# Performance work log

Hardware: AMD Instinct MI355X
Metric: run time of the kernel (lower is better)

## Reference

```python
import jax, jax.numpy as jnp
import numpy as np

GRID_SIZE = 5
SPLINE_ORDER = 3
NUM_COEFF = GRID_SIZE + SPLINE_ORDER  # 8
L = 3
B, I, H = 4096, 256, 512
EPS = 1e-5


def make_grid(in_features):
    # efficient-kan default grid over [-1, 1] extended by spline_order knots each side
    h = 2.0 / GRID_SIZE
    g = jnp.arange(-SPLINE_ORDER, GRID_SIZE + SPLINE_ORDER + 1, dtype=jnp.float32) * h - 1.0
    return jnp.broadcast_to(g, (in_features, g.shape[0]))  # (in, G+2k+1)


def b_splines(x, grid):
    # x: (B, in), grid: (in, G+2k+1) -> (B, in, G+k) via Cox-de-Boor recursion
    xg = x[..., None]
    bases = ((xg >= grid[:, :-1]) & (xg < grid[:, 1:])).astype(x.dtype)
    for j in range(1, SPLINE_ORDER + 1):
        left = (xg - grid[:, :-(j + 1)]) / (grid[:, j:-1] - grid[:, :-(j + 1)])
        right = (grid[:, j + 1:] - xg) / (grid[:, j + 1:] - grid[:, 1:-j])
        bases = left * bases[..., :-1] + right * bases[..., 1:]
    return bases


def kan_linear(x, base_w, spline_w, grid):
    # base path: SiLU(x) @ W_base^T ; spline path: sum over (in, coeff)
    base = jax.nn.silu(x) @ base_w.T
    spl = jnp.einsum('bik,oik->bo', b_splines(x, grid), spline_w)
    return base + spl


def layer_norm(x, g, b):
    mu = jnp.mean(x, axis=-1, keepdims=True)
    var = jnp.var(x, axis=-1, keepdims=True)
    return (x - mu) / jnp.sqrt(var + EPS) * g + b


def _sublayer(z_prev, wx_b, wx_s, wh_b, wh_s, hz_b, hz_s, phi_b, phi_s,
              hh_w, hh_b, ln_g, ln_b, x_t, grid_in, grid_h):
    s_t = kan_linear(x_t, wx_b, wx_s, grid_in) + kan_linear(z_prev, wh_b, wh_s, grid_h)
    o_t = kan_linear(s_t, phi_b, phi_s, grid_h)
    z_t = layer_norm(z_prev @ hh_w.T + hh_b + kan_linear(o_t, hz_b, hz_s, grid_h), ln_g, ln_b)
    return o_t, z_t


def setup_inputs() -> dict:
    key = jax.random.key(0)
    ks = jax.random.split(key, 24)
    s = 0.05  # small init to keep gates/splines in sane range
    inp = {
        'x_t': jax.random.normal(ks[0], (B, I), jnp.float32),
        'h_prev': jax.random.normal(ks[1], (B, H), jnp.float32),
        'c_prev': jax.random.normal(ks[2], (B, H), jnp.float32),
        'z_prev': jax.random.normal(ks[3], (L, B, H), jnp.float32),
        'wx_base': jax.random.normal(ks[4], (L, H, I), jnp.float32) * s,
        'wx_spline': jax.random.normal(ks[5], (L, H, I, NUM_COEFF), jnp.float32) * s,
        'wh_base': jax.random.normal(ks[6], (L, H, H), jnp.float32) * s,
        'wh_spline': jax.random.normal(ks[7], (L, H, H, NUM_COEFF), jnp.float32) * s,
        'hz_base': jax.random.normal(ks[8], (L, H, H), jnp.float32) * s,
        'hz_spline': jax.random.normal(ks[9], (L, H, H, NUM_COEFF), jnp.float32) * s,
        'phi_base': jax.random.normal(ks[10], (L, H, H), jnp.float32) * s,
        'phi_spline': jax.random.normal(ks[11], (L, H, H, NUM_COEFF), jnp.float32) * s,
        'hh_w': jax.random.normal(ks[12], (L, H, H), jnp.float32) * s,
        'hh_b': jax.random.normal(ks[13], (L, H), jnp.float32) * s,
        'ln_g': jnp.ones((L, H), jnp.float32),
        'ln_b': jnp.zeros((L, H), jnp.float32),
        'f_w': jax.random.normal(ks[14], (H, I + H), jnp.float32) * s,
        'f_b': jax.random.normal(ks[15], (H,), jnp.float32) * s,
        'i_w': jax.random.normal(ks[16], (H, I + H), jnp.float32) * s,
        'i_b': jax.random.normal(ks[17], (H,), jnp.float32) * s,
        'g_w': jax.random.normal(ks[18], (H, I + H), jnp.float32) * s,
        'g_b': jax.random.normal(ks[19], (H,), jnp.float32) * s,
        'o_w': jax.random.normal(ks[20], (H, L * H), jnp.float32) * s,
        'o_b': jax.random.normal(ks[21], (H,), jnp.float32) * s,
    }
    return inp


def reference(x_t, h_prev, c_prev, z_prev, wx_base, wx_spline, wh_base, wh_spline,
              hz_base, hz_spline, phi_base, phi_spline, hh_w, hh_b, ln_g, ln_b,
              f_w, f_b, i_w, i_b, g_w, g_b, o_w, o_b):
    grid_in = make_grid(I)
    grid_h = make_grid(H)
    cat = jnp.concatenate([x_t, h_prev], axis=-1)  # (B, I+H)
    f_t = jax.nn.sigmoid(cat @ f_w.T + f_b)
    i_t = jax.nn.sigmoid(cat @ i_w.T + i_b)
    g_t = jnp.tanh(cat @ g_w.T + g_b)
    # vmap the RKAN sublayer over the L stacked sublayers
    sub = jax.vmap(_sublayer, in_axes=(0,) * 13 + (None, None, None))
    o_all, z_all = sub(z_prev, wx_base, wx_spline, wh_base, wh_spline,
                       hz_base, hz_spline, phi_base, phi_spline,
                       hh_w, hh_b, ln_g, ln_b, x_t, grid_in, grid_h)
    # concat sublayer phi outputs: (L,B,H) -> (B, L*H)
    r_t = jnp.transpose(o_all, (1, 0, 2)).reshape(B, L * H)
    o_t = jax.nn.sigmoid(r_t @ o_w.T + o_b)
    c_t = f_t * c_prev + i_t * g_t
    h_t = o_t * jnp.tanh(c_t)
    return h_t, c_t, z_all
```

## Files before the change

kernel.cpp:

```cpp
#include <hip/hip_runtime.h>

typedef __attribute__((ext_vector_type(8))) short short8;
typedef __attribute__((ext_vector_type(4))) float floatx4;

__device__ inline short f2bf(float v) {
    unsigned u = __builtin_bit_cast(unsigned, v);
    unsigned r = (u + 0x7fffu + ((u >> 16) & 1u)) >> 16;
    return (short)r;
}
__device__ inline float bf2f(short s) {
    unsigned u = ((unsigned)(unsigned short)s) << 16;
    return __builtin_bit_cast(float, u);
}

__device__ inline void spline8(float v, short* arr) {
    float u = (v + 2.2f) * 2.5f;
    float fj = floorf(u);
    int jj = (int)fj;
    float t1 = u - fj;
    float ok = (jj >= 0 && jj <= 10) ? (1.f / 6.f) : 0.f;
    float t2 = t1 * t1, t3 = t2 * t1;
    float omt = 1.f - t1;
    short sw0 = f2bf(omt * omt * omt * ok);
    short sw1 = f2bf((3.f * t3 - 6.f * t2 + 4.f) * ok);
    short sw2 = f2bf((-3.f * t3 + 3.f * t2 + 3.f * t1 + 1.f) * ok);
    short sw3 = f2bf(t3 * ok);
#pragma unroll
    for (int s = 0; s < 8; ++s) {
        int rr = s - jj + 3;
        arr[s] = (rr == 0) ? sw0 : (rr == 1) ? sw1 : (rr == 2) ? sw2
                 : (rr == 3) ? sw3 : (short)0;
    }
}

__global__ __launch_bounds__(256) void gemm64(
    int swz,
    const short* __restrict__ A0, int lda0, long sA0, int K0,
    const short* __restrict__ W0, int ldw0, long sW0,
    const short* __restrict__ A1, int lda1, long sA1, int K1,
    const short* __restrict__ W1, int ldw1, long sW1,
    short* __restrict__ C, int ldc, long sC)
{
    __shared__ short As[64 * 32];
    __shared__ short Ws[128 * 32];
    const int t = threadIdx.x;
    int bxi = blockIdx.x, byi = blockIdx.y, bzi = blockIdx.z;
    if (swz) {
        int n = bxi + (byi << 6) + (bzi << 8);
        int k = n & 7, j = n >> 3;
        byi = j & 3;
        bxi = k * 8 + ((j >> 2) & 7);
        bzi = j >> 5;
    }
    const int z = bzi;
    const int bm = bxi * 64;
    const int bn = byi * 128;
    const int lane = t & 63, w = t >> 6;
    const int wm = (w >> 1) * 32, wn = (w & 1) * 64;
    const int lrow = lane & 15, quad = lane >> 4;

    floatx4 acc[2][4] = {};

    const short* A = A0 + (long)z * sA0;
    const short* W = W0 + (long)z * sW0;
    int K = K0, lda = lda0, ldw = ldw0;

    for (int seg = 0; seg < 2; ++seg) {
        for (int k0 = 0; k0 < K; k0 += 32) {
            {
                int row = t >> 2, cg = (t & 3) * 8;
                const short* gp = A + (long)(bm + row) * lda + k0 + cg;
                __builtin_amdgcn_global_load_lds(
                    (const __attribute__((address_space(1))) void*)gp,
                    (__attribute__((address_space(3))) void*)(As + t * 8), 16, 0, 0);
            }
#pragma unroll
            for (int j = 0; j < 2; ++j) {
                int cj = j * 256 + t;
                int row = cj >> 2, cg = (cj & 3) * 8;
                const short* gq = W + (long)(bn + row) * ldw + k0 + cg;
                __builtin_amdgcn_global_load_lds(
                    (const __attribute__((address_space(1))) void*)gq,
                    (__attribute__((address_space(3))) void*)(Ws + cj * 8), 16, 0, 0);
            }
            __syncthreads();
            short8 af[2], bfr[4];
#pragma unroll
            for (int mi = 0; mi < 2; ++mi)
                af[mi] = *(const short8*)(As + (wm + mi * 16 + lrow) * 32 + quad * 8);
#pragma unroll
            for (int ni = 0; ni < 4; ++ni)
                bfr[ni] = *(const short8*)(Ws + (wn + ni * 16 + lrow) * 32 + quad * 8);
#pragma unroll
            for (int mi = 0; mi < 2; ++mi)
#pragma unroll
                for (int ni = 0; ni < 4; ++ni)
                    acc[mi][ni] = __builtin_amdgcn_mfma_f32_16x16x32_bf16(
                        af[mi], bfr[ni], acc[mi][ni], 0, 0, 0);
            __syncthreads();
        }
        A = A1 + (long)z * sA1; W = W1 + (long)z * sW1;
        K = K1; lda = lda1; ldw = ldw1;
    }

    short* Cz = C + (long)z * sC;
#pragma unroll
    for (int mi = 0; mi < 2; ++mi)
#pragma unroll
        for (int ni = 0; ni < 4; ++ni)
#pragma unroll
            for (int r = 0; r < 4; ++r) {
                int row = bm + wm + mi * 16 + quad * 4 + r;
                int col = bn + wn + ni * 16 + lrow;
                Cz[(long)row * ldc + col] = f2bf(acc[mi][ni][r]);
            }
}

__global__ __launch_bounds__(256) void megapack(
    const float* __restrict__ wx_b, const float* __restrict__ wx_s,
    const float* __restrict__ wh_b, const float* __restrict__ wh_s,
    const float* __restrict__ hz_b, const float* __restrict__ hz_s,
    const float* __restrict__ phi_b, const float* __restrict__ phi_s,
    const float* __restrict__ hh_w, const float* __restrict__ o_w,
    const float* __restrict__ f_w, const float* __restrict__ i_w,
    const float* __restrict__ g_w,
    short* __restrict__ Wx, short* __restrict__ Wh, short* __restrict__ Whz,
    short* __restrict__ Wphi, short* __restrict__ HHb, short* __restrict__ OWb,
    short* __restrict__ Wg)
{
    int bid = blockIdx.x, tid = threadIdx.x;
    if (bid < 13824) {
        long idx = (long)bid * 256 + tid;
        int r = (int)(idx / 2304), c = (int)(idx % 2304);
        float v = (c < 256) ? wx_b[(long)r * 256 + c]
                            : wx_s[(long)r * 2048 + (c - 256)];
        Wx[idx] = f2bf(v);
    } else if (bid < 96768) {
        int jb = bid - 13824;
        int job = jb / 27648, lb = jb % 27648;
        const float* bp = (job == 0) ? wh_b : (job == 1) ? hz_b : phi_b;
        const float* sp = (job == 0) ? wh_s : (job == 1) ? hz_s : phi_s;
        short* dp = (job == 0) ? Wh : (job == 1) ? Whz : Wphi;
        long idx = (long)lb * 256 + tid;
        int r = (int)(idx / 4608), c = (int)(idx % 4608);
        float v = (c < 512) ? bp[(long)r * 512 + c]
                            : sp[(long)r * 4096 + (c - 512)];
        dp[idx] = f2bf(v);
    } else if (bid < 99840) {
        long idx = (long)(bid - 96768) * 256 + tid;
        HHb[idx] = f2bf(hh_w[idx]);
    } else if (bid < 102912) {
        long idx = (long)(bid - 99840) * 256 + tid;
        OWb[idx] = f2bf(o_w[idx]);
    } else if (bid < 104448) {
        long idx = (long)(bid - 102912) * 256 + tid;
        Wg[idx] = f2bf(f_w[idx]);
    } else if (bid < 105984) {
        long idx = (long)(bid - 104448) * 256 + tid;
        Wg[393216 + idx] = f2bf(i_w[idx]);
    } else {
        long idx = (long)(bid - 105984) * 256 + tid;
        Wg[786432 + idx] = f2bf(g_w[idx]);
    }
}

__global__ __launch_bounds__(256) void prep_acts(
    const float* __restrict__ x_t, const float* __restrict__ h_prev,
    const float* __restrict__ z_prev,
    short* __restrict__ Xe, short* __restrict__ Agate,
    short* __restrict__ Ze, short* __restrict__ zraw)
{
    int bid = blockIdx.x, tid = threadIdx.x;
    if (bid < 4096) {
        int r = bid, i = tid;
        float v = x_t[(long)r * 256 + i];
        Agate[(long)r * 768 + i] = f2bf(v);
        long ob = (long)r * 2304;
        Xe[ob + i] = f2bf(v / (1.f + __expf(-v)));
        short arr[8];
        spline8(v, arr);
        *(short8*)(Xe + ob + 256 + (long)i * 8) = *(const short8*)arr;
    } else if (bid < 12288) {
        long idx = (long)(bid - 4096) * 256 + tid;
        long b = idx >> 9; int hh = (int)(idx & 511);
        Agate[b * 768 + 256 + hh] = f2bf(h_prev[idx]);
    } else {
        int j = bid - 12288;
        int r = j >> 1, i = (j & 1) * 256 + tid;
        float v = z_prev[(long)r * 512 + i];
        zraw[(long)r * 512 + i] = f2bf(v);
        long ob = (long)r * 4608;
        Ze[ob + i] = f2bf(v / (1.f + __expf(-v)));
        short arr[8];
        spline8(v, arr);
        *(short8*)(Ze + ob + 512 + (long)i * 8) = *(const short8*)arr;
    }
}

__global__ __launch_bounds__(256) void expand_bf16_kernel(
    const short* __restrict__ x, int inF, short* __restrict__ out)
{
    int i = blockIdx.x * 256 + threadIdx.x;
    int r = blockIdx.y;
    float v = bf2f(x[(long)r * inF + i]);

    long ob = (long)r * inF * 9;
    out[ob + i] = f2bf(v / (1.f + __expf(-v)));

    short arr[8];
    spline8(v, arr);
    *(short8*)(out + ob + inF + (long)i * 8) = *(const short8*)arr;
}

__global__ __launch_bounds__(256) void ln_kernel(const short* __restrict__ zpre,
                                                 const float* __restrict__ hh_b,
                                                 const float* __restrict__ ln_g,
                                                 const float* __restrict__ ln_b,
                                                 float* __restrict__ out)
{
    int row = blockIdx.x;
    int l = row >> 12;
    int t = threadIdx.x;
    const short* x = zpre + (long)row * 512;
    float v0 = bf2f(x[t]) + hh_b[l * 512 + t];
    float v1 = bf2f(x[t + 256]) + hh_b[l * 512 + t + 256];
    float s = v0 + v1, sq = v0 * v0 + v1 * v1;
#pragma unroll
    for (int off = 32; off; off >>= 1) {
        s += __shfl_down(s, off);
        sq += __shfl_down(sq, off);
    }
    __shared__ float ls[4], lq[4];
    int w = t >> 6, lane = t & 63;
    if (lane == 0) { ls[w] = s; lq[w] = sq; }
    __syncthreads();
    float S = ls[0] + ls[1] + ls[2] + ls[3];
    float Q = lq[0] + lq[1] + lq[2] + lq[3];
    float mu = S * (1.f / 512.f);
    float var = Q * (1.f / 512.f) - mu * mu;
    float rstd = rsqrtf(var + 1e-5f);
    float* o = out + (long)row * 512;
    o[t]       = (v0 - mu) * rstd * ln_g[l * 512 + t]       + ln_b[l * 512 + t];
    o[t + 256] = (v1 - mu) * rstd * ln_g[l * 512 + t + 256] + ln_b[l * 512 + t + 256];
}

__global__ __launch_bounds__(256) void cell_epilogue(const short* __restrict__ gates,
                                                     const short* __restrict__ opre,
                                                     const float* __restrict__ c_prev,
                                                     const float* __restrict__ f_b,
                                                     const float* __restrict__ i_b,
                                                     const float* __restrict__ g_b,
                                                     const float* __restrict__ o_b,
                                                     float* __restrict__ out)
{
    long idx = blockIdx.x * 256L + threadIdx.x;
    long b = idx >> 9; int h = (int)(idx & 511);
    const short* g = gates + b * 1536;
    float fp = bf2f(g[h]) + f_b[h];
    float ip = bf2f(g[512 + h]) + i_b[h];
    float gp = bf2f(g[1024 + h]) + g_b[h];
    float op = bf2f(opre[idx]) + o_b[h];
    float ft = 1.f / (1.f + __expf(-fp));
    float it = 1.f / (1.f + __expf(-ip));
    float gt = tanhf(gp);
    float ot = 1.f / (1.f + __expf(-op));
    float c = ft * c_prev[idx] + it * gt;
    out[idx] = ot * tanhf(c);
    out[idx + 2097152] = c;
}

extern "C" void kernel_launch(void* const* d_in, const int* in_sizes, int n_in,
                              void* d_out, int out_size, void* d_ws, size_t ws_size,
                              hipStream_t stream)
{
    const float* x_t       = (const float*)d_in[0];
    const float* h_prev    = (const float*)d_in[1];
    const float* c_prev    = (const float*)d_in[2];
    const float* z_prev    = (const float*)d_in[3];
    const float* wx_base   = (const float*)d_in[4];
    const float* wx_spline = (const float*)d_in[5];
    const float* wh_base   = (const float*)d_in[6];
    const float* wh_spline = (const float*)d_in[7];
    const float* hz_base   = (const float*)d_in[8];
    const float* hz_spline = (const float*)d_in[9];
    const float* phi_base  = (const float*)d_in[10];
    const float* phi_spline= (const float*)d_in[11];
    const float* hh_w      = (const float*)d_in[12];
    const float* hh_b      = (const float*)d_in[13];
    const float* ln_g      = (const float*)d_in[14];
    const float* ln_b      = (const float*)d_in[15];
    const float* f_w       = (const float*)d_in[16];
    const float* f_b       = (const float*)d_in[17];
    const float* i_w       = (const float*)d_in[18];
    const float* i_b       = (const float*)d_in[19];
    const float* g_w       = (const float*)d_in[20];
    const float* g_b       = (const float*)d_in[21];
    const float* o_w       = (const float*)d_in[22];
    const float* o_b       = (const float*)d_in[23];
    float* out = (float*)d_out;
    const long BH = 4096L * 512;

    char* p = (char*)d_ws;
    auto alloc = [&](size_t bytes) {
        char* q = p;
        p += (bytes + 255) & ~(size_t)255;
        return q;
    };

    short* Wx   = (short*)alloc(3L * 512 * 2304 * 2);
    short* Wh   = (short*)alloc(3L * 512 * 4608 * 2);
    short* Whz  = (short*)alloc(3L * 512 * 4608 * 2);
    short* Wphi = (short*)alloc(3L * 512 * 4608 * 2);
    short* HHb  = (short*)alloc(3L * 512 * 512 * 2);
    short* OWb  = (short*)alloc(512L * 1536 * 2);
    short* Wg   = (short*)alloc(1536L * 768 * 2);
    short* Agate= (short*)alloc(4096L * 768 * 2);
    short* zraw = (short*)alloc(3L * 4096 * 512 * 2);
    short* sraw = (short*)alloc(3L * 4096 * 512 * 2);
    short* XR   = (short*)alloc(4096L * 2304 * 2);
    short* Ebuf = (short*)alloc(3L * 4096 * 4608 * 2);
    short* Xe = XR;
    short* Rbuf = XR;
    short* zpre = sraw;
    short* gbuf = Ebuf;
    short* opre = Ebuf + 4096L * 1536;

    megapack<<<107520, 256, 0, stream>>>(
        wx_base, wx_spline, wh_base, wh_spline, hz_base, hz_spline,
        phi_base, phi_spline, hh_w, o_w, f_w, i_w, g_w,
        Wx, Wh, Whz, Wphi, HHb, OWb, Wg);

    prep_acts<<<36864, 256, 0, stream>>>(x_t, h_prev, z_prev, Xe, Agate, Ebuf, zraw);

    gemm64<<<dim3(64, 4, 3), 256, 0, stream>>>(1,
        Xe, 2304, 0, 2304,                 Wx, 2304, 512L * 2304,
        Ebuf, 4608, 4096L * 4608, 4608,    Wh, 4608, 512L * 4608,
        sraw, 512, 4096L * 512);

    expand_bf16_kernel<<<dim3(2, 12288), 256, 0, stream>>>(sraw, 512, Ebuf);

    gemm64<<<dim3(64, 4, 3), 256, 0, stream>>>(1,
        Ebuf, 4608, 4096L * 4608, 4608,    Wphi, 4608, 512L * 4608,
        Ebuf, 4608, 0, 0,                  Wphi, 4608, 0,
        Rbuf, 1536, 512);

    expand_bf16_kernel<<<dim3(2, 12288), 256, 0, stream>>>(Rbuf, 512, Ebuf);

    gemm64<<<dim3(64, 4, 3), 256, 0, stream>>>(1,
        Ebuf, 13824, 4608, 4608,           Whz, 4608, 512L * 4608,
        zraw, 512, 4096L * 512, 512,       HHb, 512, 512L * 512,
        zpre, 512, 4096L * 512);

    ln_kernel<<<12288, 256, 0, stream>>>(zpre, hh_b, ln_g, ln_b, out + 2 * BH);

    gemm64<<<dim3(64, 12, 1), 256, 0, stream>>>(0,
        Agate, 768, 0, 768,  Wg, 768, 0,
        Agate, 768, 0, 0,    Wg, 768, 0,
        gbuf, 1536, 0);

    gemm64<<<dim3(64, 4, 1), 256, 0, stream>>>(0,
        Rbuf, 1536, 0, 1536, OWb, 1536, 0,
        Rbuf, 1536, 0, 0,    OWb, 1536, 0,
        opre, 512, 0);

    cell_epilogue<<<8192, 256, 0, stream>>>(gbuf, opre, c_prev, f_b, i_b, g_b, o_b, out);
}
```

Before: 826.8 us.

## Use 128x128 split-K GEMM with fp32 partials for KAN sublayer GEMMs

Replaces the 64x128-tile GEMMs for the three big sublayer GEMMs with a 128x128-tile kernel that splits K in two. Each split writes fp32 partials, and the following expand and layernorm kernels sum the two halves. Larger tiles should raise MFMA reuse per LDS load, and split-K keeps enough blocks to fill the GPU. The cost is extra fp32 partial traffic (write plus reread of two buffers), a higher register count, and loss of the old bf16 intermediate rounding.

```diff
diff --git a/kernel.cpp b/kernel.cpp
--- a/kernel.cpp
+++ b/kernel.cpp
@@ -31,6 +31,89 @@
         arr[s] = (rr == 0) ? sw0 : (rr == 1) ? sw1 : (rr == 2) ? sw2
                  : (rr == 3) ? sw3 : (short)0;
     }
+}
+
+__global__ __launch_bounds__(256, 3) void gemm128(
+    int S, int Kh,
+    const short* __restrict__ A0, int lda0, long sA0, int K0,
+    const short* __restrict__ W0, int ldw0, long sW0,
+    const short* __restrict__ A1, int lda1, long sA1, int K1,
+    const short* __restrict__ W1, int ldw1, long sW1,
+    float* __restrict__ C, int ldc, long sC, long sSplit)
+{
+    __shared__ short As[128 * 32];
+    __shared__ short Ws[128 * 32];
+    const int t = threadIdx.x;
+    int n = blockIdx.x + (blockIdx.y << 5) + (blockIdx.z << 7);
+    int k8 = n & 7, j = n >> 3;
+    int byi = j & 3;
+    int t2 = j >> 2;
+    int bxi = k8 * 4 + (t2 & 3);
+    int bzi = t2 >> 2;
+    const int z = bzi / S, s = bzi % S;
+    const int bm = bxi * 128, bn = byi * 128;
+    const int lane = t & 63, w = t >> 6;
+    const int wm = (w >> 1) * 64, wn = (w & 1) * 64;
+    const int lrow = lane & 15, quad = lane >> 4;
+
+    floatx4 acc[4][4] = {};
+
+    const int kbeg = s * Kh, kend = kbeg + Kh;
+
+    const short* A = A0 + (long)z * sA0;
+    const short* W = W0 + (long)z * sW0;
+    int lda = lda0, ldw = ldw0;
+    int kb = kbeg, ke = (kend < K0) ? kend : K0;
+
+    for (int seg = 0; seg < 2; ++seg) {
+        for (int kv = kb; kv < ke; kv += 32) {
+#pragma unroll
+            for (int cj = 0; cj < 2; ++cj) {
+                int c = cj * 256 + t;
+                int row = c >> 2, cg = (c & 3) * 8;
+                const short* gp = A + (long)(bm + row) * lda + kv + cg;
+                __builtin_amdgcn_global_load_lds(
+                    (const __attribute__((address_space(1))) void*)gp,
+                    (__attribute__((address_space(3))) void*)(As + c * 8), 16, 0, 0);
+                const short* gq = W + (long)(bn + row) * ldw + kv + cg;
+                __builtin_amdgcn_global_load_lds(
+                    (const __attribute__((address_space(1))) void*)gq,
+                    (__attribute__((address_space(3))) void*)(Ws + c * 8), 16, 0, 0);
+            }
+            __syncthreads();
+            short8 af[4], bfr[4];
+#pragma unroll
+            for (int mi = 0; mi < 4; ++mi)
+                af[mi] = *(const short8*)(As + (wm + mi * 16 + lrow) * 32 + quad * 8);
+#pragma unroll
+            for (int ni = 0; ni < 4; ++ni)
+                bfr[ni] = *(const short8*)(Ws + (wn + ni * 16 + lrow) * 32 + quad * 8);
+#pragma unroll
+            for (int mi = 0; mi < 4; ++mi)
+#pragma unroll
+                for (int ni = 0; ni < 4; ++ni)
+                    acc[mi][ni] = __builtin_amdgcn_mfma_f32_16x16x32_bf16(
+                        af[mi], bfr[ni], acc[mi][ni], 0, 0, 0);
+            __syncthreads();
+        }
+        A = A1 + (long)z * sA1;
+        W = W1 + (long)z * sW1;
+        lda = lda1; ldw = ldw1;
+        kb = ((kbeg > K0) ? kbeg : K0) - K0;
+        ke = kend - K0;
+    }
+
+    float* Cz = C + (long)z * sC + (long)s * sSplit;
+#pragma unroll
+    for (int mi = 0; mi < 4; ++mi)
+#pragma unroll
+        for (int ni = 0; ni < 4; ++ni)
+#pragma unroll
+            for (int r = 0; r < 4; ++r) {
+                int row = bm + wm + mi * 16 + quad * 4 + r;
+                int col = bn + wn + ni * 16 + lrow;
+                Cz[(long)row * ldc + col] = acc[mi][ni][r];
+            }
 }
 
 __global__ __launch_bounds__(256) void gemm64(
@@ -197,12 +280,15 @@
     }
 }
 
-__global__ __launch_bounds__(256) void expand_bf16_kernel(
-    const short* __restrict__ x, int inF, short* __restrict__ out)
+__global__ __launch_bounds__(256) void expand_pair(
+    const float* __restrict__ P, long split_off, int inF,
+    short* __restrict__ out, short* __restrict__ compact)
 {
     int i = blockIdx.x * 256 + threadIdx.x;
     int r = blockIdx.y;
-    float v = bf2f(x[(long)r * inF + i]);
+    long idx = (long)r * inF + i;
+    float v = P[idx] + P[idx + split_off];
+    if (compact) compact[idx] = f2bf(v);
 
     long ob = (long)r * inF * 9;
     out[ob + i] = f2bf(v / (1.f + __expf(-v)));
@@ -212,18 +298,19 @@
     *(short8*)(out + ob + inF + (long)i * 8) = *(const short8*)arr;
 }
 
-__global__ __launch_bounds__(256) void ln_kernel(const short* __restrict__ zpre,
-                                                 const float* __restrict__ hh_b,
-                                                 const float* __restrict__ ln_g,
-                                                 const float* __restrict__ ln_b,
-                                                 float* __restrict__ out)
+__global__ __launch_bounds__(256) void ln_pair(const float* __restrict__ P,
+                                               long split_off,
+                                               const float* __restrict__ hh_b,
+                                               const float* __restrict__ ln_g,
+                                               const float* __restrict__ ln_b,
+                                               float* __restrict__ out)
 {
     int row = blockIdx.x;
     int l = row >> 12;
     int t = threadIdx.x;
-    const short* x = zpre + (long)row * 512;
-    float v0 = bf2f(x[t]) + hh_b[l * 512 + t];
-    float v1 = bf2f(x[t + 256]) + hh_b[l * 512 + t + 256];
+    long base = (long)row * 512;
+    float v0 = P[base + t]       + P[base + t + split_off]       + hh_b[l * 512 + t];
+    float v1 = P[base + t + 256] + P[base + t + 256 + split_off] + hh_b[l * 512 + t + 256];
     float s = v0 + v1, sq = v0 * v0 + v1 * v1;
 #pragma unroll
     for (int off = 32; off; off >>= 1) {
@@ -316,14 +403,14 @@
     short* Wg   = (short*)alloc(1536L * 768 * 2);
     short* Agate= (short*)alloc(4096L * 768 * 2);
     short* zraw = (short*)alloc(3L * 4096 * 512 * 2);
-    short* sraw = (short*)alloc(3L * 4096 * 512 * 2);
     short* XR   = (short*)alloc(4096L * 2304 * 2);
     short* Ebuf = (short*)alloc(3L * 4096 * 4608 * 2);
+    float* Pbuf = (float*)alloc(2L * 3 * 4096 * 512 * 4);
     short* Xe = XR;
     short* Rbuf = XR;
-    short* zpre = sraw;
     short* gbuf = Ebuf;
     short* opre = Ebuf + 4096L * 1536;
+    const long PS = 3L * 4096 * 512;
 
     megapack<<<107520, 256, 0, stream>>>(
         wx_base, wx_spline, wh_base, wh_spline, hz_base, hz_spline,
@@ -332,26 +419,26 @@
 
     prep_acts<<<36864, 256, 0, stream>>>(x_t, h_prev, z_prev, Xe, Agate, Ebuf, zraw);
 
-    gemm64<<<dim3(64, 4, 3), 256, 0, stream>>>(1,
+    gemm128<<<dim3(32, 4, 6), 256, 0, stream>>>(2, 3456,
         Xe, 2304, 0, 2304,                 Wx, 2304, 512L * 2304,
         Ebuf, 4608, 4096L * 4608, 4608,    Wh, 4608, 512L * 4608,
-        sraw, 512, 4096L * 512);
-
-    expand_bf16_kernel<<<dim3(2, 12288), 256, 0, stream>>>(sraw, 512, Ebuf);
-
-    gemm64<<<dim3(64, 4, 3), 256, 0, stream>>>(1,
+        Pbuf, 512, 4096L * 512, PS);
+
+    expand_pair<<<dim3(2, 12288), 256, 0, stream>>>(Pbuf, PS, 512, Ebuf, (short*)0);
+
+    gemm128<<<dim3(32, 4, 6), 256, 0, stream>>>(2, 2304,
         Ebuf, 4608, 4096L * 4608, 4608,    Wphi, 4608, 512L * 4608,
-        Ebuf, 4608, 0, 0,                  Wphi, 4608, 0,
-        Rbuf, 1536, 512);
-
-    expand_bf16_kernel<<<dim3(2, 12288), 256, 0, stream>>>(Rbuf, 512, Ebuf);
-
-    gemm64<<<dim3(64, 4, 3), 256, 0, stream>>>(1,
+        zraw, 0, 0, 0,                     Wphi, 0, 0,
+        Pbuf, 1536, 512, PS);
+
+    expand_pair<<<dim3(2, 12288), 256, 0, stream>>>(Pbuf, PS, 512, Ebuf, Rbuf);
+
+    gemm128<<<dim3(32, 4, 6), 256, 0, stream>>>(2, 2560,
         Ebuf, 13824, 4608, 4608,           Whz, 4608, 512L * 4608,
         zraw, 512, 4096L * 512, 512,       HHb, 512, 512L * 512,
-        zpre, 512, 4096L * 512);
-
-    ln_kernel<<<12288, 256, 0, stream>>>(zpre, hh_b, ln_g, ln_b, out + 2 * BH);
+        Pbuf, 512, 4096L * 512, PS);
+
+    ln_pair<<<12288, 256, 0, stream>>>(Pbuf, PS, hh_b, ln_g, ln_b, out + 2 * BH);
 
     gemm64<<<dim3(64, 12, 1), 256, 0, stream>>>(0,
         Agate, 768, 0, 768,  Wg, 768, 0,
```

Result: faster. 740.8 us (-10.4%).
